# Kernel tuning notes

Hardware: AMD Instinct MI355X
Metric: run time of the kernel (lower is better)

Reference implementation:

```python
import jax, jax.numpy as jnp
import numpy as np

N, C, H, W = 16, 256, 64, 64
KC, VC, HEADS = 256, 256, 8

def setup_inputs() -> dict:
    key = jax.random.key(0)
    ks = jax.random.split(key, 9)
    s = 0.02
    return {
        "x": jax.random.normal(ks[0], (N, C, H, W), dtype=jnp.float32),
        "Wk": jax.random.normal(ks[1], (KC, C), dtype=jnp.float32) * s,
        "bk": jax.random.normal(ks[2], (KC,), dtype=jnp.float32) * s,
        "Wq": jax.random.normal(ks[3], (KC, C), dtype=jnp.float32) * s,
        "bq": jax.random.normal(ks[4], (KC,), dtype=jnp.float32) * s,
        "Wv": jax.random.normal(ks[5], (VC, C), dtype=jnp.float32) * s,
        "bv": jax.random.normal(ks[6], (VC,), dtype=jnp.float32) * s,
        "Wr": jax.random.normal(ks[7], (C, VC), dtype=jnp.float32) * s,
        "br": jax.random.normal(ks[8], (C,), dtype=jnp.float32) * s,
    }

def reference(x, Wk, bk, Wq, bq, Wv, bv, Wr, br):
    n, c, h, w = x.shape
    hw = h * w
    hk = KC // HEADS   # per-head key channels
    hv = VC // HEADS   # per-head value channels
    # 1x1 convs as channel matmuls
    keys = jnp.einsum('oi,nihw->nohw', Wk, x) + bk[None, :, None, None]
    queries = jnp.einsum('oi,nihw->nohw', Wq, x) + bq[None, :, None, None]
    values = jnp.einsum('oi,nihw->nohw', Wv, x) + bv[None, :, None, None]
    # split heads: (n, heads, ch_per_head, hw)
    k = keys.reshape(n, HEADS, hk, hw)
    q = queries.reshape(n, HEADS, hk, hw)
    v = values.reshape(n, HEADS, hv, hw)
    k = jax.nn.softmax(k, axis=3)   # softmax over spatial positions
    q = jax.nn.softmax(q, axis=2)   # softmax over key channels
    # context: (n, heads, hk, hv)
    ctx = jnp.einsum('nhkl,nhvl->nhkv', k, v)
    # attended: (n, heads, hv, hw)
    att = jnp.einsum('nhkv,nhkl->nhvl', ctx, q)
    agg = att.reshape(n, VC, h, w)
    out = jnp.einsum('ov,nvhw->nohw', Wr, agg) + br[None, :, None, None] + x
    return out
```

## Files before the change

### kernel.cpp

```cpp
#include <hip/hip_runtime.h>

#define NB   16
#define CD   256
#define HWD  4096

typedef __attribute__((ext_vector_type(8))) short short8;
typedef __attribute__((ext_vector_type(4))) float f32x4;

static __device__ __forceinline__ float b2f(unsigned short u) {
  union { unsigned int i; float f; } x; x.i = ((unsigned int)u) << 16; return x.f;
}
static __device__ __forceinline__ unsigned short f2b(float f) {
  union { float f; unsigned int i; } x; x.f = f;
  return (unsigned short)((x.i + 0x7fffu + ((x.i >> 16) & 1u)) >> 16);
}

static __device__ __forceinline__ void gload16(const void* g, const unsigned short* l) {
  __builtin_amdgcn_global_load_lds(
      (const __attribute__((address_space(1))) void*)g,
      (__attribute__((address_space(3))) void*)l, 16, 0, 0);
}

__global__ __launch_bounds__(256)
void prep_kernel(const float* __restrict__ Wk, const float* __restrict__ Wq,
                 const float* __restrict__ Wv, unsigned short* __restrict__ Wc)
{
  int e4 = blockIdx.x * 256 + threadIdx.x;
  int base = e4 * 4;
  int w = base >> 16, off = base & 65535;
  const float* W = (w == 0) ? Wk : (w == 1) ? Wq : Wv;
  f32x4 v = *(const f32x4*)(W + off);
  unsigned int lo = (unsigned int)f2b(v.x) | ((unsigned int)f2b(v.y) << 16);
  unsigned int hi = (unsigned int)f2b(v.z) | ((unsigned int)f2b(v.w) << 16);
  *(uint2*)(Wc + base) = make_uint2(lo, hi);
}

__global__ __launch_bounds__(256)
void xt_kernel(const float* __restrict__ x, unsigned short* __restrict__ xT)
{
  __shared__ __align__(16) unsigned short T[64 * 72];
  const int t = threadIdx.x;
  const int l0 = blockIdx.x * 64, c0 = blockIdx.y * 64, n = blockIdx.z;
  const int l = t & 63, cs = t >> 6;
  const float* xn = x + (size_t)n * CD * HWD;
#pragma unroll
  for (int i = 0; i < 16; ++i) {
    int c = cs + i * 4;
    T[l * 72 + c] = f2b(xn[(size_t)(c0 + c) * HWD + l0 + l]);
  }
  __syncthreads();
  unsigned short* dst = xT + ((size_t)n * HWD + l0) * CD + c0;
#pragma unroll
  for (int i = 0; i < 2; ++i) {
    int e = t + i * 256;
    int lr = e >> 3, c8 = (e & 7) * 8;
    *(short8*)(dst + (size_t)lr * CD + c8) = *(const short8*)(T + lr * 72 + c8);
  }
}

__global__ __launch_bounds__(256, 2)
void kqv_kernel(const unsigned short* __restrict__ Wc,
                const unsigned short* __restrict__ xT,
                const float* __restrict__ bk, const float* __restrict__ bq,
                const float* __restrict__ bv,
                unsigned short* __restrict__ keys,
                unsigned short* __restrict__ qsm,
                unsigned short* __restrict__ vals)
{
  __shared__ __align__(16) unsigned short smem[32768];

  const int t  = threadIdx.x;
  const int lt = blockIdx.x;
  const int mt = blockIdx.y;
  const int n  = blockIdx.z;
  const int l0 = lt * 128;
  const int m0 = mt * 128;
  const int wsel = m0 >> 8;
  const int ocbase = m0 & 255;

  const unsigned short* Ag  = Wc;
  const unsigned short* Btn = xT + (size_t)n * HWD * CD;

  const int w = t >> 6, lane = t & 63;
  const int wr = (w >> 1) * 64, wc = (w & 1) * 64;
  const int lhi = lane >> 4, llo = lane & 15;
  const int rsw = llo & 7;

  f32x4 acc[4][4] = {};

  auto stage = [&](int buf, int ks) {
    unsigned short* As = smem + buf * 16384;
    unsigned short* Bs = As + 8192;
    const int k0 = ks * 64;
#pragma unroll
    for (int i = 0; i < 4; ++i) {
      int s   = t + i * 256;
      int row = s >> 3;
      int src = ((s ^ row) & 7) << 3;
      gload16(Ag  + (size_t)(m0 + row) * CD + k0 + src, As + s * 8);
      gload16(Btn + (size_t)(l0 + row) * CD + k0 + src, Bs + s * 8);
    }
  };

  auto compute = [&](int buf) {
    const unsigned short* As = smem + buf * 16384;
    const unsigned short* Bs = As + 8192;
#pragma unroll
    for (int kk = 0; kk < 2; ++kk) {
      const int slot = (kk * 4 + lhi) ^ rsw;
      short8 a[4], b[4];
#pragma unroll
      for (int mi = 0; mi < 4; ++mi)
        a[mi] = *(const short8*)(As + (wr + mi * 16 + llo) * 64 + slot * 8);
#pragma unroll
      for (int ni = 0; ni < 4; ++ni)
        b[ni] = *(const short8*)(Bs + (wc + ni * 16 + llo) * 64 + slot * 8);
#pragma unroll
      for (int mi = 0; mi < 4; ++mi)
#pragma unroll
        for (int ni = 0; ni < 4; ++ni)
          acc[mi][ni] = __builtin_amdgcn_mfma_f32_16x16x32_bf16(a[mi], b[ni], acc[mi][ni], 0, 0, 0);
    }
  };

  stage(0, 0);
  __syncthreads();
#pragma unroll
  for (int ks = 0; ks < 4; ++ks) {
    if (ks < 3) stage((ks + 1) & 1, ks + 1);
    compute(ks & 1);
    __syncthreads();
  }

  const float* bias = (wsel == 0) ? bk : (wsel == 1) ? bq : bv;
  float breg[4][4];
#pragma unroll
  for (int mi = 0; mi < 4; ++mi)
#pragma unroll
    for (int r = 0; r < 4; ++r)
      breg[mi][r] = bias[ocbase + wr + mi * 16 + lhi * 4 + r];
#pragma unroll
  for (int mi = 0; mi < 4; ++mi)
#pragma unroll
    for (int ni = 0; ni < 4; ++ni)
#pragma unroll
      for (int r = 0; r < 4; ++r)
        acc[mi][ni][r] += breg[mi][r];

  if (wsel == 1) {
#pragma unroll
    for (int g = 0; g < 2; ++g) {
#pragma unroll
      for (int ni = 0; ni < 4; ++ni) {
        float m = -1e30f;
#pragma unroll
        for (int mi = 2 * g; mi < 2 * g + 2; ++mi)
#pragma unroll
          for (int r = 0; r < 4; ++r) m = fmaxf(m, acc[mi][ni][r]);
        m = fmaxf(m, __shfl_xor(m, 16));
        m = fmaxf(m, __shfl_xor(m, 32));
        float s = 0.f;
#pragma unroll
        for (int mi = 2 * g; mi < 2 * g + 2; ++mi)
#pragma unroll
          for (int r = 0; r < 4; ++r) {
            float e = __expf(acc[mi][ni][r] - m);
            acc[mi][ni][r] = e;
            s += e;
          }
        s += __shfl_xor(s, 16);
        s += __shfl_xor(s, 32);
        float inv = 1.f / s;
#pragma unroll
        for (int mi = 2 * g; mi < 2 * g + 2; ++mi)
#pragma unroll
          for (int r = 0; r < 4; ++r) acc[mi][ni][r] *= inv;
      }
    }
  }

  unsigned short* Co = smem;
#pragma unroll
  for (int mi = 0; mi < 4; ++mi)
#pragma unroll
    for (int ni = 0; ni < 4; ++ni) {
      int col = wc + ni * 16 + llo;
#pragma unroll
      for (int r = 0; r < 4; ++r) {
        int row = wr + mi * 16 + lhi * 4 + r;
        Co[row * 136 + col] = f2b(acc[mi][ni][r]);
      }
    }
  __syncthreads();

  unsigned short* dst = ((wsel == 0) ? keys : (wsel == 1) ? qsm : vals)
                        + ((size_t)(n * CD + ocbase)) * HWD + l0;
#pragma unroll
  for (int i = 0; i < 8; ++i) {
    int e = t + i * 256;
    int row = e >> 4, c8 = (e & 15) * 8;
    *(short8*)(dst + (size_t)row * HWD + c8) = *(const short8*)(Co + row * 136 + c8);
  }
}

__global__ __launch_bounds__(256)
void rowstats_kernel(const unsigned short* __restrict__ keys,
                     float* __restrict__ stats)
{
  __shared__ float red[8];
  const int r = blockIdx.x;
  const int t = threadIdx.x;
  const unsigned short* rowp = keys + (size_t)r * HWD;
  float v[16];
  float m = -1e30f;
#pragma unroll
  for (int i = 0; i < 2; ++i) {
    const short8 u = *(const short8*)(rowp + t * 8 + i * 2048);
#pragma unroll
    for (int j = 0; j < 8; ++j) {
      v[i * 8 + j] = b2f((unsigned short)u[j]);
      m = fmaxf(m, v[i * 8 + j]);
    }
  }
#pragma unroll
  for (int off = 1; off < 64; off <<= 1) m = fmaxf(m, __shfl_xor(m, off));
  if ((t & 63) == 0) red[t >> 6] = m;
  __syncthreads();
  m = fmaxf(fmaxf(red[0], red[1]), fmaxf(red[2], red[3]));
  float s = 0.f;
#pragma unroll
  for (int i = 0; i < 16; ++i) s += __expf(v[i] - m);
#pragma unroll
  for (int off = 1; off < 64; off <<= 1) s += __shfl_xor(s, off);
  if ((t & 63) == 0) red[4 + (t >> 6)] = s;
  __syncthreads();
  if (t == 0) {
    s = red[4] + red[5] + red[6] + red[7];
    stats[r * 2]     = m;
    stats[r * 2 + 1] = 1.f / s;
  }
}

__global__ __launch_bounds__(256)
void ctx_kernel(const unsigned short* __restrict__ keys,
                const unsigned short* __restrict__ vals,
                const float* __restrict__ stats,
                float* __restrict__ ctxp)
{
  __shared__ float Cs[4][32][33];
  const int hf = blockIdx.x;
  const int nh = blockIdx.y;
  const int n = nh >> 3, h = nh & 7;
  const int t = threadIdx.x, w = t >> 6, lane = t & 63;
  const int lhi = lane >> 4, llo = lane & 15;
  const int lbase = hf * 2048 + w * 512;

  const unsigned short* kr = keys + (size_t)(n * CD + h * 32) * HWD;
  const unsigned short* vr = vals + (size_t)(n * CD + h * 32) * HWD;

  float mx[2], inv[2];
#pragma unroll
  for (int mi = 0; mi < 2; ++mi) {
    int kc = mi * 16 + llo;
    mx[mi]  = stats[(n * CD + h * 32 + kc) * 2];
    inv[mi] = stats[(n * CD + h * 32 + kc) * 2 + 1];
  }

  f32x4 acc[2][2] = {};
  for (int ks = 0; ks < 16; ++ks) {
    const int loff = lbase + ks * 32 + lhi * 8;
    short8 a[2], b[2];
#pragma unroll
    for (int mi = 0; mi < 2; ++mi) {
      const short8 u = *(const short8*)(kr + (size_t)(mi * 16 + llo) * HWD + loff);
      short8 af;
#pragma unroll
      for (int j = 0; j < 8; ++j)
        af[j] = (short)f2b(__expf(b2f((unsigned short)u[j]) - mx[mi]) * inv[mi]);
      a[mi] = af;
    }
#pragma unroll
    for (int ni = 0; ni < 2; ++ni)
      b[ni] = *(const short8*)(vr + (size_t)(ni * 16 + llo) * HWD + loff);
    acc[0][0] = __builtin_amdgcn_mfma_f32_16x16x32_bf16(a[0], b[0], acc[0][0], 0, 0, 0);
    acc[0][1] = __builtin_amdgcn_mfma_f32_16x16x32_bf16(a[0], b[1], acc[0][1], 0, 0, 0);
    acc[1][0] = __builtin_amdgcn_mfma_f32_16x16x32_bf16(a[1], b[0], acc[1][0], 0, 0, 0);
    acc[1][1] = __builtin_amdgcn_mfma_f32_16x16x32_bf16(a[1], b[1], acc[1][1], 0, 0, 0);
  }

#pragma unroll
  for (int mi = 0; mi < 2; ++mi)
#pragma unroll
    for (int ni = 0; ni < 2; ++ni)
#pragma unroll
      for (int r = 0; r < 4; ++r)
        Cs[w][mi * 16 + lhi * 4 + r][ni * 16 + llo] = acc[mi][ni][r];
  __syncthreads();
#pragma unroll
  for (int i = 0; i < 4; ++i) {
    int e = t + i * 256;
    int kc = e >> 5, vc = e & 31;
    float sum = Cs[0][kc][vc] + Cs[1][kc][vc] + Cs[2][kc][vc] + Cs[3][kc][vc];
    ctxp[((size_t)hf * 128 + nh) * 1024 + e] = sum;
  }
}

__global__ __launch_bounds__(256)
void proj_kernel(const float* __restrict__ ctxp, const float* __restrict__ Wr,
                 unsigned short* __restrict__ M)
{
  __shared__ float cs[32][33];
  const int nh = blockIdx.x;
  const int n = nh >> 3, h = nh & 7;
  const int t = threadIdx.x;
#pragma unroll
  for (int i = 0; i < 4; ++i) {
    int e = t + i * 256;
    cs[e >> 5][e & 31] = ctxp[(size_t)nh * 1024 + e] + ctxp[((size_t)128 + nh) * 1024 + e];
  }
  __syncthreads();
  float wreg[32];
  const float* wp = Wr + (size_t)t * 256 + h * 32;
#pragma unroll
  for (int i = 0; i < 8; ++i) {
    f32x4 v = *(const f32x4*)(wp + i * 4);
    wreg[i * 4] = v.x; wreg[i * 4 + 1] = v.y; wreg[i * 4 + 2] = v.z; wreg[i * 4 + 3] = v.w;
  }
  unsigned short o16[32];
#pragma unroll
  for (int kc = 0; kc < 32; ++kc) {
    float s = 0.f;
#pragma unroll
    for (int vv = 0; vv < 32; ++vv) s += wreg[vv] * cs[kc][vv];
    o16[kc] = f2b(s);
  }
  unsigned short* mp = M + (size_t)(n * CD + t) * 256 + h * 32;
#pragma unroll
  for (int i = 0; i < 8; ++i) {
    unsigned int lo = (unsigned int)o16[i * 4]     | ((unsigned int)o16[i * 4 + 1] << 16);
    unsigned int hi = (unsigned int)o16[i * 4 + 2] | ((unsigned int)o16[i * 4 + 3] << 16);
    *(uint2*)(mp + i * 4) = make_uint2(lo, hi);
  }
}

__global__ __launch_bounds__(256, 2)
void out_kernel(const unsigned short* __restrict__ M,
                const unsigned short* __restrict__ qsm,
                const float* __restrict__ br,
                const float* __restrict__ x,
                float* __restrict__ out)
{
  __shared__ __align__(16) unsigned short As[64 * 264];
  __shared__ __align__(16) unsigned short Bs[64 * 264];
  const int t = threadIdx.x;
  const int lt = blockIdx.x, mt = blockIdx.y, n = blockIdx.z;
  const int l0 = lt * 64, m0 = mt * 64;

  const unsigned short* Mn = M + (size_t)n * CD * 256;
#pragma unroll
  for (int i = 0; i < 8; ++i) {
    int idx = t + i * 256;
    int row = idx >> 5, s8 = (idx & 31) << 3;
    *(short8*)(As + row * 264 + s8) = *(const short8*)(Mn + (size_t)(m0 + row) * 256 + s8);
  }
  const unsigned short* qn = qsm + (size_t)n * CD * HWD;
  {
    int l = t & 63, g0 = t >> 6;
#pragma unroll
    for (int i = 0; i < 16; ++i) {
      int c = (g0 + i * 4) << 2;
      unsigned short q0 = qn[(size_t)(c + 0) * HWD + l0 + l];
      unsigned short q1 = qn[(size_t)(c + 1) * HWD + l0 + l];
      unsigned short q2 = qn[(size_t)(c + 2) * HWD + l0 + l];
      unsigned short q3 = qn[(size_t)(c + 3) * HWD + l0 + l];
      unsigned int lo = (unsigned int)q0 | ((unsigned int)q1 << 16);
      unsigned int hi = (unsigned int)q2 | ((unsigned int)q3 << 16);
      *(uint2*)(Bs + l * 264 + c) = make_uint2(lo, hi);
    }
  }
  __syncthreads();

  const int w = t >> 6, lane = t & 63;
  const int wr = (w >> 1) * 32, wc = (w & 1) * 32;
  const int lhi = lane >> 4, llo = lane & 15;

  f32x4 acc[2][2] = {};
#pragma unroll
  for (int kk = 0; kk < 8; ++kk) {
    const int koff = kk * 32 + lhi * 8;
    short8 a0 = *(const short8*)(As + (wr + llo) * 264 + koff);
    short8 a1 = *(const short8*)(As + (wr + 16 + llo) * 264 + koff);
    short8 b0 = *(const short8*)(Bs + (wc + llo) * 264 + koff);
    short8 b1 = *(const short8*)(Bs + (wc + 16 + llo) * 264 + koff);
    acc[0][0] = __builtin_amdgcn_mfma_f32_16x16x32_bf16(a0, b0, acc[0][0], 0, 0, 0);
    acc[0][1] = __builtin_amdgcn_mfma_f32_16x16x32_bf16(a0, b1, acc[0][1], 0, 0, 0);
    acc[1][0] = __builtin_amdgcn_mfma_f32_16x16x32_bf16(a1, b0, acc[1][0], 0, 0, 0);
    acc[1][1] = __builtin_amdgcn_mfma_f32_16x16x32_bf16(a1, b1, acc[1][1], 0, 0, 0);
  }
  __syncthreads();

  float* Qs = (float*)As;
#pragma unroll
  for (int mi = 0; mi < 2; ++mi)
#pragma unroll
    for (int ni = 0; ni < 2; ++ni)
#pragma unroll
      for (int r = 0; r < 4; ++r) {
        int row = wr + mi * 16 + lhi * 4 + r;
        int col = wc + ni * 16 + llo;
        Qs[row * 65 + col] = acc[mi][ni][r] + br[m0 + row];
      }
  __syncthreads();

  const float* xn = x + (size_t)n * CD * HWD;
  {
    int l = t & 63, r0 = t >> 6;
#pragma unroll
    for (int i = 0; i < 16; ++i) {
      int row = r0 + i * 4;
      size_t off = (size_t)(m0 + row) * HWD + l0 + l;
      out[(size_t)n * CD * HWD + off] = Qs[row * 65 + l] + xn[off];
    }
  }
}

extern "C" void kernel_launch(void* const* d_in, const int* in_sizes, int n_in,
                              void* d_out, int out_size, void* d_ws, size_t ws_size,
                              hipStream_t stream) {
  const float* x  = (const float*)d_in[0];
  const float* Wk = (const float*)d_in[1];
  const float* bk = (const float*)d_in[2];
  const float* Wq = (const float*)d_in[3];
  const float* bq = (const float*)d_in[4];
  const float* Wv = (const float*)d_in[5];
  const float* bv = (const float*)d_in[6];
  const float* Wr = (const float*)d_in[7];
  const float* br = (const float*)d_in[8];
  float* out = (float*)d_out;

  char* ws = (char*)d_ws;
  unsigned short* keys = (unsigned short*)(ws);
  unsigned short* vals = (unsigned short*)(ws + 33554432);
  unsigned short* qsm  = (unsigned short*)(ws + 67108864);
  float* stats         = (float*)(ws + 100663296);
  float* ctxp          = (float*)(ws + 100696064);
  unsigned short* M    = (unsigned short*)(ws + 101744640);
  unsigned short* Wc   = (unsigned short*)(ws + 103841792);
  unsigned short* xT   = (unsigned short*)d_out;

  hipLaunchKernelGGL(prep_kernel, dim3(192), dim3(256), 0, stream, Wk, Wq, Wv, Wc);
  hipLaunchKernelGGL(xt_kernel, dim3(64, 4, NB), dim3(256), 0, stream, x, xT);
  hipLaunchKernelGGL(kqv_kernel, dim3(32, 6, NB), dim3(256), 0, stream,
                     Wc, xT, bk, bq, bv, keys, qsm, vals);
  hipLaunchKernelGGL(rowstats_kernel, dim3(NB * CD), dim3(256), 0, stream, keys, stats);
  hipLaunchKernelGGL(ctx_kernel, dim3(2, 128), dim3(256), 0, stream,
                     keys, vals, stats, ctxp);
  hipLaunchKernelGGL(proj_kernel, dim3(128), dim3(256), 0, stream, ctxp, Wr, M);
  hipLaunchKernelGGL(out_kernel, dim3(64, 4, NB), dim3(256), 0, stream,
                     M, qsm, br, x, out);
}
```

Baseline: 130.9 us.

## Store softmaxed queries transposed and rewrite output GEMM as pipelined 128x128 tiles

The query projection now writes its softmaxed output in a position-major (transposed) layout. This lets the final output kernel use the same double-buffered, direct-to-LDS 128x128 MFMA GEMM as the projection kernel, replacing the scalar strided gathers it used before. The projection kernel's K-step shrinks to 32 so LDS per block drops, and occupancy is raised to 4 blocks. The transpose kernel now uses vectorized float4 loads with a different LDS padding. The risks are that the output epilogue writes directly from MFMA fragments with only partial coalescing, and that the extra K iterations add more barriers.

```diff
diff --git a/kernel.cpp b/kernel.cpp
--- a/kernel.cpp
+++ b/kernel.cpp
@@ -38,15 +38,19 @@
 __global__ __launch_bounds__(256)
 void xt_kernel(const float* __restrict__ x, unsigned short* __restrict__ xT)
 {
-  __shared__ __align__(16) unsigned short T[64 * 72];
+  __shared__ __align__(16) unsigned short T[64 * 80];
   const int t = threadIdx.x;
   const int l0 = blockIdx.x * 64, c0 = blockIdx.y * 64, n = blockIdx.z;
-  const int l = t & 63, cs = t >> 6;
   const float* xn = x + (size_t)n * CD * HWD;
 #pragma unroll
-  for (int i = 0; i < 16; ++i) {
-    int c = cs + i * 4;
-    T[l * 72 + c] = f2b(xn[(size_t)(c0 + c) * HWD + l0 + l]);
+  for (int i = 0; i < 4; ++i) {
+    int idx = t + i * 256;
+    int c = idx >> 4, l4 = (idx & 15) * 4;
+    f32x4 v = *(const f32x4*)(xn + (size_t)(c0 + c) * HWD + l0 + l4);
+    T[(l4 + 0) * 80 + c] = f2b(v.x);
+    T[(l4 + 1) * 80 + c] = f2b(v.y);
+    T[(l4 + 2) * 80 + c] = f2b(v.z);
+    T[(l4 + 3) * 80 + c] = f2b(v.w);
   }
   __syncthreads();
   unsigned short* dst = xT + ((size_t)n * HWD + l0) * CD + c0;
@@ -54,20 +58,20 @@
   for (int i = 0; i < 2; ++i) {
     int e = t + i * 256;
     int lr = e >> 3, c8 = (e & 7) * 8;
-    *(short8*)(dst + (size_t)lr * CD + c8) = *(const short8*)(T + lr * 72 + c8);
-  }
-}
-
-__global__ __launch_bounds__(256, 2)
+    *(short8*)(dst + (size_t)lr * CD + c8) = *(const short8*)(T + lr * 80 + c8);
+  }
+}
+
+__global__ __launch_bounds__(256, 4)
 void kqv_kernel(const unsigned short* __restrict__ Wc,
                 const unsigned short* __restrict__ xT,
                 const float* __restrict__ bk, const float* __restrict__ bq,
                 const float* __restrict__ bv,
                 unsigned short* __restrict__ keys,
-                unsigned short* __restrict__ qsm,
+                unsigned short* __restrict__ qsmT,
                 unsigned short* __restrict__ vals)
 {
-  __shared__ __align__(16) unsigned short smem[32768];
+  __shared__ __align__(16) unsigned short smem[17408];
 
   const int t  = threadIdx.x;
   const int lt = blockIdx.x;
@@ -84,68 +88,60 @@
   const int w = t >> 6, lane = t & 63;
   const int wr = (w >> 1) * 64, wc = (w & 1) * 64;
   const int lhi = lane >> 4, llo = lane & 15;
-  const int rsw = llo & 7;
 
   f32x4 acc[4][4] = {};
 
   auto stage = [&](int buf, int ks) {
-    unsigned short* As = smem + buf * 16384;
-    unsigned short* Bs = As + 8192;
-    const int k0 = ks * 64;
-#pragma unroll
-    for (int i = 0; i < 4; ++i) {
+    unsigned short* As = smem + buf * 8192;
+    unsigned short* Bs = As + 4096;
+    const int k0 = ks * 32;
+#pragma unroll
+    for (int i = 0; i < 2; ++i) {
       int s   = t + i * 256;
-      int row = s >> 3;
-      int src = ((s ^ row) & 7) << 3;
+      int row = s >> 2;
+      int src = (((s ^ row) & 3)) << 3;
       gload16(Ag  + (size_t)(m0 + row) * CD + k0 + src, As + s * 8);
       gload16(Btn + (size_t)(l0 + row) * CD + k0 + src, Bs + s * 8);
     }
   };
 
   auto compute = [&](int buf) {
-    const unsigned short* As = smem + buf * 16384;
-    const unsigned short* Bs = As + 8192;
-#pragma unroll
-    for (int kk = 0; kk < 2; ++kk) {
-      const int slot = (kk * 4 + lhi) ^ rsw;
-      short8 a[4], b[4];
-#pragma unroll
-      for (int mi = 0; mi < 4; ++mi)
-        a[mi] = *(const short8*)(As + (wr + mi * 16 + llo) * 64 + slot * 8);
+    const unsigned short* As = smem + buf * 8192;
+    const unsigned short* Bs = As + 4096;
+    const int slot = (lhi ^ (llo & 3)) * 8;
+    short8 a[4], b[4];
+#pragma unroll
+    for (int mi = 0; mi < 4; ++mi)
+      a[mi] = *(const short8*)(As + (wr + mi * 16 + llo) * 32 + slot);
+#pragma unroll
+    for (int ni = 0; ni < 4; ++ni)
+      b[ni] = *(const short8*)(Bs + (wc + ni * 16 + llo) * 32 + slot);
+#pragma unroll
+    for (int mi = 0; mi < 4; ++mi)
 #pragma unroll
       for (int ni = 0; ni < 4; ++ni)
-        b[ni] = *(const short8*)(Bs + (wc + ni * 16 + llo) * 64 + slot * 8);
-#pragma unroll
-      for (int mi = 0; mi < 4; ++mi)
-#pragma unroll
-        for (int ni = 0; ni < 4; ++ni)
-          acc[mi][ni] = __builtin_amdgcn_mfma_f32_16x16x32_bf16(a[mi], b[ni], acc[mi][ni], 0, 0, 0);
-    }
+        acc[mi][ni] = __builtin_amdgcn_mfma_f32_16x16x32_bf16(a[mi], b[ni], acc[mi][ni], 0, 0, 0);
   };
 
   stage(0, 0);
   __syncthreads();
 #pragma unroll
-  for (int ks = 0; ks < 4; ++ks) {
-    if (ks < 3) stage((ks + 1) & 1, ks + 1);
+  for (int ks = 0; ks < 8; ++ks) {
+    if (ks < 7) stage((ks + 1) & 1, ks + 1);
     compute(ks & 1);
     __syncthreads();
   }
 
   const float* bias = (wsel == 0) ? bk : (wsel == 1) ? bq : bv;
-  float breg[4][4];
-#pragma unroll
-  for (int mi = 0; mi < 4; ++mi)
-#pragma unroll
-    for (int r = 0; r < 4; ++r)
-      breg[mi][r] = bias[ocbase + wr + mi * 16 + lhi * 4 + r];
-#pragma unroll
-  for (int mi = 0; mi < 4; ++mi)
-#pragma unroll
-    for (int ni = 0; ni < 4; ++ni)
-#pragma unroll
-      for (int r = 0; r < 4; ++r)
-        acc[mi][ni][r] += breg[mi][r];
+#pragma unroll
+  for (int mi = 0; mi < 4; ++mi) {
+#pragma unroll
+    for (int r = 0; r < 4; ++r) {
+      float bb = bias[ocbase + wr + mi * 16 + lhi * 4 + r];
+#pragma unroll
+      for (int ni = 0; ni < 4; ++ni) acc[mi][ni][r] += bb;
+    }
+  }
 
   if (wsel == 1) {
 #pragma unroll
@@ -177,29 +173,48 @@
           for (int r = 0; r < 4; ++r) acc[mi][ni][r] *= inv;
       }
     }
-  }
-
-  unsigned short* Co = smem;
-#pragma unroll
-  for (int mi = 0; mi < 4; ++mi)
-#pragma unroll
-    for (int ni = 0; ni < 4; ++ni) {
-      int col = wc + ni * 16 + llo;
-#pragma unroll
-      for (int r = 0; r < 4; ++r) {
-        int row = wr + mi * 16 + lhi * 4 + r;
-        Co[row * 136 + col] = f2b(acc[mi][ni][r]);
+    unsigned short* Co2 = smem;
+#pragma unroll
+    for (int mi = 0; mi < 4; ++mi)
+#pragma unroll
+      for (int ni = 0; ni < 4; ++ni) {
+        int col = wc + ni * 16 + llo;
+#pragma unroll
+        for (int r = 0; r < 4; ++r) {
+          int row = wr + mi * 16 + lhi * 4 + r;
+          Co2[col * 136 + row] = f2b(acc[mi][ni][r]);
+        }
       }
-    }
-  __syncthreads();
-
-  unsigned short* dst = ((wsel == 0) ? keys : (wsel == 1) ? qsm : vals)
-                        + ((size_t)(n * CD + ocbase)) * HWD + l0;
-#pragma unroll
-  for (int i = 0; i < 8; ++i) {
-    int e = t + i * 256;
-    int row = e >> 4, c8 = (e & 15) * 8;
-    *(short8*)(dst + (size_t)row * HWD + c8) = *(const short8*)(Co + row * 136 + c8);
+    __syncthreads();
+    unsigned short* dst = qsmT + ((size_t)n * HWD + l0) * CD + ocbase;
+#pragma unroll
+    for (int i = 0; i < 8; ++i) {
+      int e = t + i * 256;
+      int l = e >> 4, c8 = (e & 15) * 8;
+      *(short8*)(dst + (size_t)l * CD + c8) = *(const short8*)(Co2 + l * 136 + c8);
+    }
+  } else {
+    unsigned short* Co = smem;
+#pragma unroll
+    for (int mi = 0; mi < 4; ++mi)
+#pragma unroll
+      for (int ni = 0; ni < 4; ++ni) {
+        int col = wc + ni * 16 + llo;
+#pragma unroll
+        for (int r = 0; r < 4; ++r) {
+          int row = wr + mi * 16 + lhi * 4 + r;
+          Co[row * 136 + col] = f2b(acc[mi][ni][r]);
+        }
+      }
+    __syncthreads();
+    unsigned short* dst = ((wsel == 0) ? keys : vals)
+                          + ((size_t)(n * CD + (wsel == 0 ? ocbase : ocbase))) * HWD + l0;
+#pragma unroll
+    for (int i = 0; i < 8; ++i) {
+      int e = t + i * 256;
+      int row = e >> 4, c8 = (e & 15) * 8;
+      *(short8*)(dst + (size_t)row * HWD + c8) = *(const short8*)(Co + row * 136 + c8);
+    }
   }
 }
 
@@ -343,85 +358,86 @@
   }
 }
 
-__global__ __launch_bounds__(256, 2)
+__global__ __launch_bounds__(256, 4)
 void out_kernel(const unsigned short* __restrict__ M,
-                const unsigned short* __restrict__ qsm,
+                const unsigned short* __restrict__ qsmT,
                 const float* __restrict__ br,
                 const float* __restrict__ x,
                 float* __restrict__ out)
 {
-  __shared__ __align__(16) unsigned short As[64 * 264];
-  __shared__ __align__(16) unsigned short Bs[64 * 264];
+  __shared__ __align__(16) unsigned short smem[16384];
+
   const int t = threadIdx.x;
-  const int lt = blockIdx.x, mt = blockIdx.y, n = blockIdx.z;
-  const int l0 = lt * 64, m0 = mt * 64;
-
-  const unsigned short* Mn = M + (size_t)n * CD * 256;
-#pragma unroll
-  for (int i = 0; i < 8; ++i) {
-    int idx = t + i * 256;
-    int row = idx >> 5, s8 = (idx & 31) << 3;
-    *(short8*)(As + row * 264 + s8) = *(const short8*)(Mn + (size_t)(m0 + row) * 256 + s8);
-  }
-  const unsigned short* qn = qsm + (size_t)n * CD * HWD;
-  {
-    int l = t & 63, g0 = t >> 6;
-#pragma unroll
-    for (int i = 0; i < 16; ++i) {
-      int c = (g0 + i * 4) << 2;
-      unsigned short q0 = qn[(size_t)(c + 0) * HWD + l0 + l];
-      unsigned short q1 = qn[(size_t)(c + 1) * HWD + l0 + l];
-      unsigned short q2 = qn[(size_t)(c + 2) * HWD + l0 + l];
-      unsigned short q3 = qn[(size_t)(c + 3) * HWD + l0 + l];
-      unsigned int lo = (unsigned int)q0 | ((unsigned int)q1 << 16);
-      unsigned int hi = (unsigned int)q2 | ((unsigned int)q3 << 16);
-      *(uint2*)(Bs + l * 264 + c) = make_uint2(lo, hi);
-    }
-  }
-  __syncthreads();
+  const int lt = blockIdx.x;
+  const int mt = blockIdx.y;
+  const int n  = blockIdx.z;
+  const int l0 = lt * 128, m0 = mt * 128;
+
+  const unsigned short* Ag  = M + (size_t)n * CD * 256;
+  const unsigned short* Btn = qsmT + (size_t)n * HWD * CD;
 
   const int w = t >> 6, lane = t & 63;
-  const int wr = (w >> 1) * 32, wc = (w & 1) * 32;
+  const int wr = (w >> 1) * 64, wc = (w & 1) * 64;
   const int lhi = lane >> 4, llo = lane & 15;
 
-  f32x4 acc[2][2] = {};
-#pragma unroll
-  for (int kk = 0; kk < 8; ++kk) {
-    const int koff = kk * 32 + lhi * 8;
-    short8 a0 = *(const short8*)(As + (wr + llo) * 264 + koff);
-    short8 a1 = *(const short8*)(As + (wr + 16 + llo) * 264 + koff);
-    short8 b0 = *(const short8*)(Bs + (wc + llo) * 264 + koff);
-    short8 b1 = *(const short8*)(Bs + (wc + 16 + llo) * 264 + koff);
-    acc[0][0] = __builtin_amdgcn_mfma_f32_16x16x32_bf16(a0, b0, acc[0][0], 0, 0, 0);
-    acc[0][1] = __builtin_amdgcn_mfma_f32_16x16x32_bf16(a0, b1, acc[0][1], 0, 0, 0);
-    acc[1][0] = __builtin_amdgcn_mfma_f32_16x16x32_bf16(a1, b0, acc[1][0], 0, 0, 0);
-    acc[1][1] = __builtin_amdgcn_mfma_f32_16x16x32_bf16(a1, b1, acc[1][1], 0, 0, 0);
-  }
-  __syncthreads();
-
-  float* Qs = (float*)As;
-#pragma unroll
-  for (int mi = 0; mi < 2; ++mi)
-#pragma unroll
-    for (int ni = 0; ni < 2; ++ni)
-#pragma unroll
-      for (int r = 0; r < 4; ++r) {
-        int row = wr + mi * 16 + lhi * 4 + r;
-        int col = wc + ni * 16 + llo;
-        Qs[row * 65 + col] = acc[mi][ni][r] + br[m0 + row];
+  f32x4 acc[4][4] = {};
+
+  auto stage = [&](int buf, int ks) {
+    unsigned short* As = smem + buf * 8192;
+    unsigned short* Bs = As + 4096;
+    const int k0 = ks * 32;
+#pragma unroll
+    for (int i = 0; i < 2; ++i) {
+      int s   = t + i * 256;
+      int row = s >> 2;
+      int src = (((s ^ row) & 3)) << 3;
+      gload16(Ag  + (size_t)(m0 + row) * CD + k0 + src, As + s * 8);
+      gload16(Btn + (size_t)(l0 + row) * CD + k0 + src, Bs + s * 8);
+    }
+  };
+
+  auto compute = [&](int buf) {
+    const unsigned short* As = smem + buf * 8192;
+    const unsigned short* Bs = As + 4096;
+    const int slot = (lhi ^ (llo & 3)) * 8;
+    short8 a[4], b[4];
+#pragma unroll
+    for (int mi = 0; mi < 4; ++mi)
+      a[mi] = *(const short8*)(As + (wr + mi * 16 + llo) * 32 + slot);
+#pragma unroll
+    for (int ni = 0; ni < 4; ++ni)
+      b[ni] = *(const short8*)(Bs + (wc + ni * 16 + llo) * 32 + slot);
+#pragma unroll
+    for (int mi = 0; mi < 4; ++mi)
+#pragma unroll
+      for (int ni = 0; ni < 4; ++ni)
+        acc[mi][ni] = __builtin_amdgcn_mfma_f32_16x16x32_bf16(a[mi], b[ni], acc[mi][ni], 0, 0, 0);
+  };
+
+  stage(0, 0);
+  __syncthreads();
+#pragma unroll
+  for (int ks = 0; ks < 8; ++ks) {
+    if (ks < 7) stage((ks + 1) & 1, ks + 1);
+    compute(ks & 1);
+    __syncthreads();
+  }
+
+  const float* xn = x + (size_t)n * CD * HWD;
+  float* on = out + (size_t)n * CD * HWD;
+#pragma unroll
+  for (int mi = 0; mi < 4; ++mi)
+#pragma unroll
+    for (int r = 0; r < 4; ++r) {
+      int row = m0 + wr + mi * 16 + lhi * 4 + r;
+      float bb = br[row];
+#pragma unroll
+      for (int ni = 0; ni < 4; ++ni) {
+        int col = l0 + wc + ni * 16 + llo;
+        size_t off = (size_t)row * HWD + col;
+        on[off] = acc[mi][ni][r] + bb + xn[off];
       }
-  __syncthreads();
-
-  const float* xn = x + (size_t)n * CD * HWD;
-  {
-    int l = t & 63, r0 = t >> 6;
-#pragma unroll
-    for (int i = 0; i < 16; ++i) {
-      int row = r0 + i * 4;
-      size_t off = (size_t)(m0 + row) * HWD + l0 + l;
-      out[(size_t)n * CD * HWD + off] = Qs[row * 65 + l] + xn[off];
-    }
-  }
+    }
 }
 
 extern "C" void kernel_launch(void* const* d_in, const int* in_sizes, int n_in,
@@ -441,7 +457,7 @@
   char* ws = (char*)d_ws;
   unsigned short* keys = (unsigned short*)(ws);
   unsigned short* vals = (unsigned short*)(ws + 33554432);
-  unsigned short* qsm  = (unsigned short*)(ws + 67108864);
+  unsigned short* qsmT = (unsigned short*)(ws + 67108864);
   float* stats         = (float*)(ws + 100663296);
   float* ctxp          = (float*)(ws + 100696064);
   unsigned short* M    = (unsigned short*)(ws + 101744640);
@@ -451,11 +467,11 @@
   hipLaunchKernelGGL(prep_kernel, dim3(192), dim3(256), 0, stream, Wk, Wq, Wv, Wc);
   hipLaunchKernelGGL(xt_kernel, dim3(64, 4, NB), dim3(256), 0, stream, x, xT);
   hipLaunchKernelGGL(kqv_kernel, dim3(32, 6, NB), dim3(256), 0, stream,
-                     Wc, xT, bk, bq, bv, keys, qsm, vals);
+                     Wc, xT, bk, bq, bv, keys, qsmT, vals);
   hipLaunchKernelGGL(rowstats_kernel, dim3(NB * CD), dim3(256), 0, stream, keys, stats);
   hipLaunchKernelGGL(ctx_kernel, dim3(2, 128), dim3(256), 0, stream,
                      keys, vals, stats, ctxp);
   hipLaunchKernelGGL(proj_kernel, dim3(128), dim3(256), 0, stream, ctxp, Wr, M);
-  hipLaunchKernelGGL(out_kernel, dim3(64, 4, NB), dim3(256), 0, stream,
-                     M, qsm, br, x, out);
-}
+  hipLaunchKernelGGL(out_kernel, dim3(32, 2, NB), dim3(256), 0, stream,
+                     M, qsmT, br, x, out);
+}
```

Measured after the change: 144.2 us. 1.1x slower.
